# Performance work log

Measured on AMD Instinct MI355X. Metric: run time of the kernel, lower is better.

The kernel has to match this reference:

```python
import jax, jax.numpy as jnp
import numpy as np

MIN_SCALE = 0.05
MAX_SCALE = 0.2
EPS = 0.001
RATE = 4
SUBSAMPLE = 3


def box_filter(x, k):
    # matches torch: pad (1+p) before / p after on H and W, double cumsum + subtract
    if k % 2 == 0:
        k = k + 1
    p = k // 2
    xp = jnp.pad(x, ((0, 0), (0, 0), (1 + p, p), (1 + p, p)))
    c = jnp.cumsum(xp, axis=2)
    y = c[:, :, k:, :] - c[:, :, :-k, :]
    c2 = jnp.cumsum(y, axis=3)
    return c2[:, :, :, k:] - c2[:, :, :, :-k]


def _resize(x, h, w):
    # torch F.interpolate(mode='bilinear', align_corners=False) == jax bilinear, no antialias
    n, c = x.shape[0], x.shape[1]
    return jax.image.resize(x, (n, c, h, w), method='bilinear', antialias=False)


def rf_norm(x):
    N, C, H, W = x.shape
    scale = MAX_SCALE
    it = 1
    while True:  # loop bounds depend only on static config -> Python loop is jit-safe
        win = int(max(H, W) * scale)
        if win < 3 and it == 1:
            mean = x.mean(axis=(1, 2, 3), keepdims=True)
            std = x.std(axis=(1, 2, 3), ddof=1, keepdims=True) + EPS
            x = x / std - mean / std
        else:
            if SUBSAMPLE > 1 and min(H, W) > SUBSAMPLE * 10 and win > SUBSAMPLE * 5:
                xs = _resize(x, H // SUBSAMPLE, W // SUBSAMPLE)
                win = win // SUBSAMPLE
            else:
                xs = x
            h, w = xs.shape[2], xs.shape[3]
            ones = jnp.ones((1, 1, h, w), x.dtype)
            M = box_filter(ones, win)
            x_mean = box_filter(xs, win).mean(axis=1, keepdims=True) / M
            x2_mean = box_filter(xs ** 2, win).mean(axis=1, keepdims=True) / M
            var = jnp.clip(x2_mean - x_mean ** 2, 0.0) + EPS
            std = jnp.sqrt(var)
            a = 1.0 / std
            b = -x_mean / std
            mean_a = box_filter(a, win) / M
            mean_b = box_filter(b, win) / M
            if SUBSAMPLE > 1:
                mean_a = _resize(mean_a, H, W)
                mean_b = _resize(mean_b, H, W)
            x = mean_a * x + mean_b
        it += 1
        scale /= RATE  # coarse_to_fine=True
        if scale < MIN_SCALE:
            break
    return x


def setup_inputs() -> dict:
    key = jax.random.key(0)
    x = jax.random.normal(key, (16, 3, 768, 768), dtype=jnp.float32)
    return {"x": x}


def reference(x):
    return rf_norm(x)
```

## Files before the change

### kernel.cpp

```cpp
#include <hip/hip_runtime.h>


#define N_B 16
#define CCH 3
#define HF 768
#define HL 256
#define SLICE (HL * HL)
#define TOT_L (N_B * SLICE)
#define EPSV 1e-3f

__device__ __forceinline__ int cnt(int i, int P) {
  int hi = i + P; if (hi > HL - 1) hi = HL - 1;
  int lo = i - P; if (lo < 0) lo = 0;
  return hi - lo + 1;
}

__device__ __forceinline__ void scan2g(float a, float b, int g, int j,
    float2 (*s)[HL], float2 (*wt)[4]) {
  int lane = j & 63, w = j >> 6;
  __syncthreads();
#pragma unroll
  for (int d = 1; d < 64; d <<= 1) {
    float ta = __shfl_up(a, (unsigned)d);
    float tb = __shfl_up(b, (unsigned)d);
    if (lane >= d) { a += ta; b += tb; }
  }
  if (lane == 63) wt[g][w] = make_float2(a, b);
  __syncthreads();
  float offa = 0.f, offb = 0.f;
  for (int ww = 0; ww < w; ++ww) { float2 t = wt[g][ww]; offa += t.x; offb += t.y; }
  s[g][j] = make_float2(a + offa, b + offb);
  __syncthreads();
}

template <int P>
__device__ __forceinline__ float2 boxr(const float2 (*s)[HL], int g, int j) {
  int hi = j + P; if (hi > HL - 1) hi = HL - 1;
  int lo = j - P - 1;
  float2 r = s[g][hi];
  if (lo >= 0) { float2 l = s[g][lo]; r.x -= l.x; r.y -= l.y; }
  return r;
}

template <int P>
__device__ __forceinline__ void xpose_store(const float2 (*s)[HL], int tid,
    float2* __restrict__ dst, size_t nb, int col0) {
  if (tid < HL) {
    float2 r0 = boxr<P>(s, 0, tid);
    float2 r1 = boxr<P>(s, 1, tid);
    float2 r2 = boxr<P>(s, 2, tid);
    float2 r3 = boxr<P>(s, 3, tid);
    float4* d = (float4*)(dst + nb + (size_t)tid * HL + col0);
    d[0] = make_float4(r0.x, r0.y, r1.x, r1.y);
    d[1] = make_float4(r2.x, r2.y, r3.x, r3.y);
  }
}

__global__ __launch_bounds__(1024) void k1(const float* __restrict__ x,
    float2* __restrict__ UV, float2* __restrict__ Spk) {
  __shared__ float stage[4][HF];
  __shared__ float2 s[4][HL];
  __shared__ float2 wt[4][4];
  int b = blockIdx.x;
  int n = b >> 6;
  int ib = (b & 63) << 2;
  int tid = threadIdx.x;
  int g = tid >> 8, j = tid & 255;
  int srow = tid / 192, scol = (tid % 192) * 4;
  float ua = 0.f, va = 0.f;
  const size_t imgbase = (size_t)n * CCH * HF * HF;
  for (int c = 0; c < CCH; ++c) {
    __syncthreads();
    if (tid < 768) {
      const float* src = x + imgbase + (size_t)c * HF * HF
                       + (size_t)(3 * (ib + srow) + 1) * HF + scol;
      *(float4*)&stage[srow][scol] = *(const float4*)src;
    }
    __syncthreads();
    float val = stage[g][3 * j + 1];
    ua += val;
    va += val * val;
  }
  float uu = ua * (1.f / 3.f), vv = va * (1.f / 3.f);
  size_t nb = (size_t)n * SLICE;
  UV[nb + (size_t)(ib + g) * HL + j] = make_float2(uu, vv);
  scan2g(uu, vv, g, j, s, wt);
  xpose_store<25>(s, tid, Spk, nb, ib);
}

__global__ __launch_bounds__(1024) void k2(const float2* __restrict__ Spk,
    float2* __restrict__ Ppk) {
  __shared__ float2 s[4][HL];
  __shared__ float2 wt[4][4];
  int n = blockIdx.x >> 6, strip = blockIdx.x & 63;
  int tid = threadIdx.x, g = tid >> 8, j = tid & 255;
  int c = strip * 4 + g;
  size_t nb = (size_t)n * SLICE;
  float2 sv = Spk[nb + (size_t)c * HL + j];
  scan2g(sv.x, sv.y, g, j, s, wt);
  float2 bu = boxr<25>(s, g, j);
  float invM = 1.f / ((float)cnt(j, 25) * (float)cnt(c, 25));
  float xm = bu.x * invM, x2m = bu.y * invM;
  float var = x2m - xm * xm; if (var < 0.f) var = 0.f;
  float inv = 1.f / sqrtf(var + EPSV);
  scan2g(inv, -xm * inv, g, j, s, wt);
  xpose_store<25>(s, tid, Ppk, nb, strip * 4);
}

__global__ __launch_bounds__(1024) void k3(const float2* __restrict__ Ppk,
    const float2* __restrict__ UV, float2* __restrict__ AB1,
    float2* __restrict__ Qpk) {
  __shared__ float2 s[4][HL];
  __shared__ float2 wt[4][4];
  int n = blockIdx.x >> 6, strip = blockIdx.x & 63;
  int tid = threadIdx.x, g = tid >> 8, j = tid & 255;
  int i = strip * 4 + g;
  size_t nb = (size_t)n * SLICE;
  size_t idx = nb + (size_t)i * HL + j;
  float2 pv = Ppk[idx];
  scan2g(pv.x, pv.y, g, j, s, wt);
  float2 bb = boxr<25>(s, g, j);
  float invM = 1.f / ((float)cnt(i, 25) * (float)cnt(j, 25));
  float Av = bb.x * invM, Bv = bb.y * invM;
  AB1[idx] = make_float2(Av, Bv);
  float2 uv = UV[idx];
  float u2 = Av * uv.x + Bv;
  float v2 = Av * Av * uv.y + 2.f * Av * Bv * uv.x + Bv * Bv;
  scan2g(u2, v2, g, j, s, wt);
  xpose_store<6>(s, tid, Qpk, nb, strip * 4);
}

__global__ __launch_bounds__(1024) void k4(const float2* __restrict__ Qpk,
    float2* __restrict__ Rpk) {
  __shared__ float2 s[4][HL];
  __shared__ float2 wt[4][4];
  int n = blockIdx.x >> 6, strip = blockIdx.x & 63;
  int tid = threadIdx.x, g = tid >> 8, j = tid & 255;
  int c = strip * 4 + g;
  size_t nb = (size_t)n * SLICE;
  float2 qv = Qpk[nb + (size_t)c * HL + j];
  scan2g(qv.x, qv.y, g, j, s, wt);
  float2 bu = boxr<6>(s, g, j);
  float invM = 1.f / ((float)cnt(j, 6) * (float)cnt(c, 6));
  float xm = bu.x * invM, x2m = bu.y * invM;
  float var = x2m - xm * xm; if (var < 0.f) var = 0.f;
  float inv = 1.f / sqrtf(var + EPSV);
  scan2g(inv, -xm * inv, g, j, s, wt);
  xpose_store<6>(s, tid, Rpk, nb, strip * 4);
}

__device__ __forceinline__ void upw(int q, int& i0, int& i1, float& w1) {
  int d = q / 3;
  int r = q - 3 * d;
  if (r == 1) { i0 = d; i1 = d; w1 = 0.f; }
  else if (r == 2) { i0 = d; i1 = d + 1; if (i1 > HL - 1) i1 = HL - 1; w1 = 1.f / 3.f; }
  else { i1 = d; i0 = d - 1; if (i0 < 0) i0 = 0; w1 = 2.f / 3.f; }
}

__global__ __launch_bounds__(256) void k_final(
    const float* __restrict__ x, const float2* __restrict__ AB1,
    const float2* __restrict__ Rpk, float* __restrict__ out) {
  __shared__ float2 ry01[HL], ry23[HL];
  __shared__ float2 s[1][HL];
  __shared__ float2 wt[1][4];
  int nb_ = blockIdx.x;
  int y = nb_ % HF;
  int n = nb_ / HF;
  int t = threadIdx.x;
  int iy0, iy1;
  float wy1;
  upw(y, iy0, iy1, wy1);
  float wy0 = 1.f - wy1;
  size_t mb = (size_t)n * SLICE;
  float2 a0 = AB1[mb + (size_t)iy0 * HL + t];
  float2 a1 = AB1[mb + (size_t)iy1 * HL + t];
  ry01[t] = make_float2(wy0 * a0.x + wy1 * a1.x, wy0 * a0.y + wy1 * a1.y);
  float cj6 = (float)cnt(t, 6);
  float2 r0v = Rpk[mb + (size_t)iy0 * HL + t];
  scan2g(r0v.x, r0v.y, 0, t, s, wt);
  float2 b0 = boxr<6>(s, 0, t);
  float inv0 = 1.f / ((float)cnt(iy0, 6) * cj6);
  float A20 = b0.x * inv0, B20 = b0.y * inv0;
  float2 r1v = Rpk[mb + (size_t)iy1 * HL + t];
  scan2g(r1v.x, r1v.y, 0, t, s, wt);
  float2 b1 = boxr<6>(s, 0, t);
  float inv1 = 1.f / ((float)cnt(iy1, 6) * cj6);
  ry23[t] = make_float2(wy0 * A20 + wy1 * b1.x * inv1,
                        wy0 * B20 + wy1 * b1.y * inv1);
  __syncthreads();
  if (t < 192) {
    float A1c[4], B1c[4], A2c[4], B2c[4];
#pragma unroll
    for (int e = 0; e < 4; ++e) {
      int q = 4 * t + e;
      int ix0, ix1;
      float wx1;
      upw(q, ix0, ix1, wx1);
      float wx0 = 1.f - wx1;
      float2 m0 = ry01[ix0], m1 = ry01[ix1];
      float2 m2 = ry23[ix0], m3 = ry23[ix1];
      A1c[e] = wx0 * m0.x + wx1 * m1.x;
      B1c[e] = wx0 * m0.y + wx1 * m1.y;
      A2c[e] = wx0 * m2.x + wx1 * m3.x;
      B2c[e] = wx0 * m2.y + wx1 * m3.y;
    }
    size_t rowbase = ((size_t)(n * CCH) * HF + y) * HF + 4 * t;
#pragma unroll
    for (int c = 0; c < CCH; ++c) {
      const float4 xin = *(const float4*)(x + rowbase + (size_t)c * HF * HF);
      float4 o;
      o.x = A2c[0] * (A1c[0] * xin.x + B1c[0]) + B2c[0];
      o.y = A2c[1] * (A1c[1] * xin.y + B1c[1]) + B2c[1];
      o.z = A2c[2] * (A1c[2] * xin.z + B1c[2]) + B2c[2];
      o.w = A2c[3] * (A1c[3] * xin.w + B1c[3]) + B2c[3];
      *(float4*)(out + rowbase + (size_t)c * HF * HF) = o;
    }
  }
}

extern "C" void kernel_launch(void* const* d_in, const int* in_sizes, int n_in,
                              void* d_out, int out_size, void* d_ws, size_t ws_size,
                              hipStream_t stream) {
  const float* x = (const float*)d_in[0];
  float* out = (float*)d_out;
  const size_t S = (size_t)TOT_L;
  float2 *UV, *Spk, *Ppk, *AB1, *Rpk, *Qpk;
  if (ws_size >= 10 * S * sizeof(float)) {
    float2* w = (float2*)d_ws;
    UV = w; Spk = UV + S; Ppk = Spk + S; AB1 = Ppk + S; Rpk = AB1 + S;
  } else {
    AB1 = (float2*)d_ws; Rpk = AB1 + S;
    UV = (float2*)out; Spk = UV + S; Ppk = Spk + S;
  }
  Qpk = Spk;

  k1<<<N_B * 64, 1024, 0, stream>>>(x, UV, Spk);
  k2<<<N_B * 64, 1024, 0, stream>>>(Spk, Ppk);
  k3<<<N_B * 64, 1024, 0, stream>>>(Ppk, UV, AB1, Qpk);
  k4<<<N_B * 64, 1024, 0, stream>>>(Qpk, Rpk);
  k_final<<<N_B * HF, 256, 0, stream>>>(x, AB1, Rpk, out);
}
```

Measured before the change: 99.11 us.

## Drop leading barrier in scan via double-buffered LDS, skip redundant row scan

Removes the leading __syncthreads in scan2g by giving consecutive scans separate shared buffers (A/B), so each kernel avoids one or two block barriers. k1 now reads the three channel samples directly from global memory instead of staging full rows through LDS, which drops two barriers and the redundant row loads. k_final skips the second row scan when the vertical upsample weight is zero, covering one in three output rows. The cost is more LDS per block, and the direct strided loads in k1 are uncoalesced.

```diff
diff --git a/kernel.cpp b/kernel.cpp
--- a/kernel.cpp
+++ b/kernel.cpp
@@ -18,7 +18,6 @@
 __device__ __forceinline__ void scan2g(float a, float b, int g, int j,
     float2 (*s)[HL], float2 (*wt)[4]) {
   int lane = j & 63, w = j >> 6;
-  __syncthreads();
 #pragma unroll
   for (int d = 1; d < 64; d <<= 1) {
     float ta = __shfl_up(a, (unsigned)d);
@@ -58,95 +57,83 @@
 
 __global__ __launch_bounds__(1024) void k1(const float* __restrict__ x,
     float2* __restrict__ UV, float2* __restrict__ Spk) {
-  __shared__ float stage[4][HF];
-  __shared__ float2 s[4][HL];
-  __shared__ float2 wt[4][4];
+  __shared__ float2 sA[4][HL];
+  __shared__ float2 wtA[4][4];
   int b = blockIdx.x;
   int n = b >> 6;
   int ib = (b & 63) << 2;
   int tid = threadIdx.x;
   int g = tid >> 8, j = tid & 255;
-  int srow = tid / 192, scol = (tid % 192) * 4;
-  float ua = 0.f, va = 0.f;
-  const size_t imgbase = (size_t)n * CCH * HF * HF;
-  for (int c = 0; c < CCH; ++c) {
-    __syncthreads();
-    if (tid < 768) {
-      const float* src = x + imgbase + (size_t)c * HF * HF
-                       + (size_t)(3 * (ib + srow) + 1) * HF + scol;
-      *(float4*)&stage[srow][scol] = *(const float4*)src;
-    }
-    __syncthreads();
-    float val = stage[g][3 * j + 1];
-    ua += val;
-    va += val * val;
-  }
-  float uu = ua * (1.f / 3.f), vv = va * (1.f / 3.f);
+  const float* xp = x + (size_t)n * CCH * HF * HF
+                  + (size_t)(3 * (ib + g) + 1) * HF + (3 * j + 1);
+  float c0 = xp[0], c1 = xp[HF * HF], c2 = xp[2 * HF * HF];
+  float uu = (c0 + c1 + c2) * (1.f / 3.f);
+  float vv = (c0 * c0 + c1 * c1 + c2 * c2) * (1.f / 3.f);
   size_t nb = (size_t)n * SLICE;
   UV[nb + (size_t)(ib + g) * HL + j] = make_float2(uu, vv);
-  scan2g(uu, vv, g, j, s, wt);
-  xpose_store<25>(s, tid, Spk, nb, ib);
+  scan2g(uu, vv, g, j, sA, wtA);
+  xpose_store<25>(sA, tid, Spk, nb, ib);
 }
 
 __global__ __launch_bounds__(1024) void k2(const float2* __restrict__ Spk,
     float2* __restrict__ Ppk) {
-  __shared__ float2 s[4][HL];
-  __shared__ float2 wt[4][4];
+  __shared__ float2 sA[4][HL], sB[4][HL];
+  __shared__ float2 wtA[4][4], wtB[4][4];
   int n = blockIdx.x >> 6, strip = blockIdx.x & 63;
   int tid = threadIdx.x, g = tid >> 8, j = tid & 255;
   int c = strip * 4 + g;
   size_t nb = (size_t)n * SLICE;
   float2 sv = Spk[nb + (size_t)c * HL + j];
-  scan2g(sv.x, sv.y, g, j, s, wt);
-  float2 bu = boxr<25>(s, g, j);
+  scan2g(sv.x, sv.y, g, j, sA, wtA);
+  float2 bu = boxr<25>(sA, g, j);
   float invM = 1.f / ((float)cnt(j, 25) * (float)cnt(c, 25));
   float xm = bu.x * invM, x2m = bu.y * invM;
   float var = x2m - xm * xm; if (var < 0.f) var = 0.f;
   float inv = 1.f / sqrtf(var + EPSV);
-  scan2g(inv, -xm * inv, g, j, s, wt);
-  xpose_store<25>(s, tid, Ppk, nb, strip * 4);
+  scan2g(inv, -xm * inv, g, j, sB, wtB);
+  xpose_store<25>(sB, tid, Ppk, nb, strip * 4);
 }
 
 __global__ __launch_bounds__(1024) void k3(const float2* __restrict__ Ppk,
     const float2* __restrict__ UV, float2* __restrict__ AB1,
     float2* __restrict__ Qpk) {
-  __shared__ float2 s[4][HL];
-  __shared__ float2 wt[4][4];
+  __shared__ float2 sA[4][HL], sB[4][HL];
+  __shared__ float2 wtA[4][4], wtB[4][4];
   int n = blockIdx.x >> 6, strip = blockIdx.x & 63;
   int tid = threadIdx.x, g = tid >> 8, j = tid & 255;
   int i = strip * 4 + g;
   size_t nb = (size_t)n * SLICE;
   size_t idx = nb + (size_t)i * HL + j;
   float2 pv = Ppk[idx];
-  scan2g(pv.x, pv.y, g, j, s, wt);
-  float2 bb = boxr<25>(s, g, j);
+  scan2g(pv.x, pv.y, g, j, sA, wtA);
+  float2 bb = boxr<25>(sA, g, j);
   float invM = 1.f / ((float)cnt(i, 25) * (float)cnt(j, 25));
   float Av = bb.x * invM, Bv = bb.y * invM;
   AB1[idx] = make_float2(Av, Bv);
   float2 uv = UV[idx];
   float u2 = Av * uv.x + Bv;
   float v2 = Av * Av * uv.y + 2.f * Av * Bv * uv.x + Bv * Bv;
-  scan2g(u2, v2, g, j, s, wt);
-  xpose_store<6>(s, tid, Qpk, nb, strip * 4);
+  scan2g(u2, v2, g, j, sB, wtB);
+  xpose_store<6>(sB, tid, Qpk, nb, strip * 4);
 }
 
 __global__ __launch_bounds__(1024) void k4(const float2* __restrict__ Qpk,
     float2* __restrict__ Rpk) {
-  __shared__ float2 s[4][HL];
-  __shared__ float2 wt[4][4];
+  __shared__ float2 sA[4][HL], sB[4][HL];
+  __shared__ float2 wtA[4][4], wtB[4][4];
   int n = blockIdx.x >> 6, strip = blockIdx.x & 63;
   int tid = threadIdx.x, g = tid >> 8, j = tid & 255;
   int c = strip * 4 + g;
   size_t nb = (size_t)n * SLICE;
   float2 qv = Qpk[nb + (size_t)c * HL + j];
-  scan2g(qv.x, qv.y, g, j, s, wt);
-  float2 bu = boxr<6>(s, g, j);
+  scan2g(qv.x, qv.y, g, j, sA, wtA);
+  float2 bu = boxr<6>(sA, g, j);
   float invM = 1.f / ((float)cnt(j, 6) * (float)cnt(c, 6));
   float xm = bu.x * invM, x2m = bu.y * invM;
   float var = x2m - xm * xm; if (var < 0.f) var = 0.f;
   float inv = 1.f / sqrtf(var + EPSV);
-  scan2g(inv, -xm * inv, g, j, s, wt);
-  xpose_store<6>(s, tid, Rpk, nb, strip * 4);
+  scan2g(inv, -xm * inv, g, j, sB, wtB);
+  xpose_store<6>(sB, tid, Rpk, nb, strip * 4);
 }
 
 __device__ __forceinline__ void upw(int q, int& i0, int& i1, float& w1) {
@@ -161,8 +148,8 @@
     const float* __restrict__ x, const float2* __restrict__ AB1,
     const float2* __restrict__ Rpk, float* __restrict__ out) {
   __shared__ float2 ry01[HL], ry23[HL];
-  __shared__ float2 s[1][HL];
-  __shared__ float2 wt[1][4];
+  __shared__ float2 sA[1][HL], sB[1][HL];
+  __shared__ float2 wtA[1][4], wtB[1][4];
   int nb_ = blockIdx.x;
   int y = nb_ % HF;
   int n = nb_ / HF;
@@ -177,16 +164,20 @@
   ry01[t] = make_float2(wy0 * a0.x + wy1 * a1.x, wy0 * a0.y + wy1 * a1.y);
   float cj6 = (float)cnt(t, 6);
   float2 r0v = Rpk[mb + (size_t)iy0 * HL + t];
-  scan2g(r0v.x, r0v.y, 0, t, s, wt);
-  float2 b0 = boxr<6>(s, 0, t);
+  scan2g(r0v.x, r0v.y, 0, t, sA, wtA);
+  float2 b0 = boxr<6>(sA, 0, t);
   float inv0 = 1.f / ((float)cnt(iy0, 6) * cj6);
   float A20 = b0.x * inv0, B20 = b0.y * inv0;
-  float2 r1v = Rpk[mb + (size_t)iy1 * HL + t];
-  scan2g(r1v.x, r1v.y, 0, t, s, wt);
-  float2 b1 = boxr<6>(s, 0, t);
-  float inv1 = 1.f / ((float)cnt(iy1, 6) * cj6);
-  ry23[t] = make_float2(wy0 * A20 + wy1 * b1.x * inv1,
-                        wy0 * B20 + wy1 * b1.y * inv1);
+  if (wy1 == 0.f) {
+    ry23[t] = make_float2(A20, B20);
+  } else {
+    float2 r1v = Rpk[mb + (size_t)iy1 * HL + t];
+    scan2g(r1v.x, r1v.y, 0, t, sB, wtB);
+    float2 b1 = boxr<6>(sB, 0, t);
+    float inv1 = 1.f / ((float)cnt(iy1, 6) * cj6);
+    ry23[t] = make_float2(wy0 * A20 + wy1 * b1.x * inv1,
+                          wy0 * B20 + wy1 * b1.y * inv1);
+  }
   __syncthreads();
   if (t < 192) {
     float A1c[4], B1c[4], A2c[4], B2c[4];
```

Result: faster. 96.19 us (median of 2 runs) (-3.0%).
